# Performance work log

Hardware: AMD Instinct MI355X
Metric: run time of the kernel (lower is better)

The kernel has to match this reference:

```python
import jax, jax.numpy as jnp
import numpy as np

D_MODEL = 512
NHEAD = 8
MAX_REL = 256  # max_relative_position


def _linear(x, w, b):
    # torch nn.Linear: y = x @ W^T + b, W: [out, in]
    return jnp.einsum('...i,oi->...o', x, w) + b


def setup_inputs() -> dict:
    key = jax.random.key(0)
    ks = jax.random.split(key, 16)
    B, S, D = 32, 512, D_MODEL
    s = 0.02
    inp = {
        'query': jax.random.normal(ks[0], (B, S, D), jnp.float32),
        'key':   jax.random.normal(ks[1], (B, S, D), jnp.float32),
        'value': jax.random.normal(ks[2], (B, S, D), jnp.float32),
        # local attention projections (torch Linear weights [out,in])
        'wq': jax.random.normal(ks[3], (D, D), jnp.float32) * s,
        'bq': jnp.zeros((D,), jnp.float32),
        'wk': jax.random.normal(ks[4], (D, D), jnp.float32) * s,
        'bk': jnp.zeros((D,), jnp.float32),
        'wv': jax.random.normal(ks[5], (D, D), jnp.float32) * s,
        'bv': jnp.zeros((D,), jnp.float32),
        'wo': jax.random.normal(ks[6], (D, D), jnp.float32) * s,
        'bo': jnp.zeros((D,), jnp.float32),
        # relative-position key embedding table [2*MAX_REL+1, head_dim]
        'rel_k': jax.random.normal(ks[7], (2 * MAX_REL + 1, D // NHEAD), jnp.float32) * s,
        # global nn.MultiheadAttention (nhead//2 heads): packed in_proj + out_proj
        'g_in_w': jax.random.normal(ks[8], (3 * D, D), jnp.float32) * s,
        'g_in_b': jnp.zeros((3 * D,), jnp.float32),
        'g_out_w': jax.random.normal(ks[9], (D, D), jnp.float32) * s,
        'g_out_b': jnp.zeros((D,), jnp.float32),
    }
    return inp


def reference(query, key, value, wq, bq, wk, bk, wv, bv, wo, bo, rel_k,
              g_in_w, g_in_b, g_out_w, g_out_b):
    B, S, D = query.shape
    H, hd = NHEAD, D // NHEAD

    # --- local attention with relative-position bias ---
    q = _linear(query, wq, bq).reshape(B, S, H, hd).transpose(0, 2, 1, 3)  # [B,H,S,hd]
    k = _linear(key,   wk, bk).reshape(B, S, H, hd).transpose(0, 2, 1, 3)
    v = _linear(value, wv, bv).reshape(B, S, H, hd).transpose(0, 2, 1, 3)

    scores = jnp.einsum('bhqd,bhkd->bhqk', q, k) / jnp.sqrt(jnp.float32(hd))

    # relative positions: distance[i,j] = j - i, clamped, shifted to [0, 2*MAX_REL]
    idx = jnp.arange(S)
    rel_ids = jnp.clip(idx[None, :] - idx[:, None], -MAX_REL, MAX_REL) + MAX_REL  # [S,S]
    rel_pos_k = rel_k[rel_ids]  # [S, S, hd]
    scores = scores + jnp.einsum('bhld,lrd->bhlr', q, rel_pos_k)

    attn = jax.nn.softmax(scores, axis=-1)
    local = jnp.einsum('bhqk,bhkd->bhqd', attn, v)
    local = local.transpose(0, 2, 1, 3).reshape(B, S, D)

    # --- global MHA with H//2 heads ---
    Hg = H // 2
    hdg = D // Hg
    qg = _linear(query, g_in_w[:D], g_in_b[:D]).reshape(B, S, Hg, hdg).transpose(0, 2, 1, 3)
    kg = _linear(key,   g_in_w[D:2 * D], g_in_b[D:2 * D]).reshape(B, S, Hg, hdg).transpose(0, 2, 1, 3)
    vg = _linear(value, g_in_w[2 * D:], g_in_b[2 * D:]).reshape(B, S, Hg, hdg).transpose(0, 2, 1, 3)
    gs = jnp.einsum('bhqd,bhkd->bhqk', qg, kg) / jnp.sqrt(jnp.float32(hdg))
    ga = jax.nn.softmax(gs, axis=-1)
    g = jnp.einsum('bhqk,bhkd->bhqd', ga, vg).transpose(0, 2, 1, 3).reshape(B, S, D)
    g = _linear(g, g_out_w, g_out_b)

    combined = 0.7 * local + 0.3 * g
    return _linear(combined, wo, bo)
```

## Files before the change

kernel.cpp:

```cpp
#include <hip/hip_runtime.h>

typedef __attribute__((ext_vector_type(8))) short bh8;
typedef __attribute__((ext_vector_type(4))) float f4;

#define DEVI static __device__ __forceinline__

DEVI unsigned short f2b(float f) {
  union { float f; unsigned u; } v; v.f = f;
  unsigned r = v.u + 0x7fffu + ((v.u >> 16) & 1u);
  return (unsigned short)(r >> 16);
}
DEVI float b2f(unsigned short h) {
  union { unsigned u; float f; } v; v.u = ((unsigned)h) << 16;
  return v.f;
}
DEVI f4 mfma16(bh8 a, bh8 b, f4 c) {
  return __builtin_amdgcn_mfma_f32_16x16x32_bf16(a, b, c, 0, 0, 0);
}
DEVI void gload_lds16(const unsigned short* g, unsigned short* l) {
  __builtin_amdgcn_global_load_lds(
      (const __attribute__((address_space(1))) void*)(g),
      (__attribute__((address_space(3))) void*)(l), 16, 0, 0);
}

__global__ __launch_bounds__(256) void prep_x_kern(
    const float* __restrict__ q, const float* __restrict__ k, const float* __restrict__ v,
    unsigned short* __restrict__ xq, unsigned short* __restrict__ xk, unsigned short* __restrict__ xv) {
  long i = ((long)blockIdx.x * 256 + threadIdx.x) * 4;
  if (i >= 8388608L) return;
  float4 a = *(const float4*)(q + i);
  float4 b = *(const float4*)(k + i);
  float4 c = *(const float4*)(v + i);
  union { unsigned short s[4]; uint2 u; } pa, pb, pc;
  pa.s[0] = f2b(a.x); pa.s[1] = f2b(a.y); pa.s[2] = f2b(a.z); pa.s[3] = f2b(a.w);
  pb.s[0] = f2b(b.x); pb.s[1] = f2b(b.y); pb.s[2] = f2b(b.z); pb.s[3] = f2b(b.w);
  pc.s[0] = f2b(c.x); pc.s[1] = f2b(c.y); pc.s[2] = f2b(c.z); pc.s[3] = f2b(c.w);
  *(uint2*)(xq + i) = pa.u;
  *(uint2*)(xk + i) = pb.u;
  *(uint2*)(xv + i) = pc.u;
}

__global__ __launch_bounds__(256) void prep_w_kern(
    const float* __restrict__ wq, const float* __restrict__ wk, const float* __restrict__ wv,
    const float* __restrict__ g_in_w, const float* __restrict__ g_out_w,
    const float* __restrict__ wo, const float* __restrict__ rel_k,
    unsigned short* __restrict__ Wq, unsigned short* __restrict__ Wk, unsigned short* __restrict__ Wv,
    unsigned short* __restrict__ Wgo, unsigned short* __restrict__ Wo_, unsigned short* __restrict__ Rk) {
  long i = ((long)blockIdx.x * 256 + threadIdx.x) * 4;
  if (i >= 2129984L) return;
  const float* src; unsigned short* dst; long off;
  if (i < 524288L)        { dst = Wq;  off = i; src = (i < 262144L) ? wq + i : g_in_w + (i - 262144L); }
  else if (i < 1048576L)  { long j = i - 524288L;  dst = Wk;  off = j; src = (j < 262144L) ? wk + j : g_in_w + j; }
  else if (i < 1572864L)  { long j = i - 1048576L; dst = Wv;  off = j; src = (j < 262144L) ? wv + j : g_in_w + 262144L + j; }
  else if (i < 1835008L)  { long j = i - 1572864L; dst = Wgo; off = j; src = g_out_w + j; }
  else if (i < 2097152L)  { long j = i - 1835008L; dst = Wo_; off = j; src = wo + j; }
  else                    { long j = i - 2097152L; dst = Rk;  off = j; src = rel_k + j; }
  float4 f = *(const float4*)src;
  union { unsigned short s[4]; uint2 u; } p;
  p.s[0] = f2b(f.x); p.s[1] = f2b(f.y); p.s[2] = f2b(f.z); p.s[3] = f2b(f.w);
  *(uint2*)(dst + off) = p.u;
}

template <int NB, int EPI>
__global__ __launch_bounds__(256) void gemm_bf16_kern(
    const unsigned short* __restrict__ A, const unsigned short* __restrict__ Bw,
    const float* __restrict__ bias0, const float* __restrict__ bias1,
    const unsigned short* __restrict__ aux,
    unsigned short* __restrict__ outb, unsigned short* __restrict__ outb2,
    float* __restrict__ outf) {
  __shared__ unsigned short lsA[128 * 32];
  __shared__ unsigned short lsB[128 * 32];
  const int t = threadIdx.x;
  const int lane = t & 63, w = t >> 6;
  const int l15 = lane & 15, g8 = (lane >> 4) * 8, g4 = (lane >> 4) * 4;
  int n = blockIdx.x;
  int x = n >> 3, c = n & 7;
  const int rb = (c * 16 + (x & 15)) * 128;
  const int cb = (x >> 4) * 128;
  const int wr = (w >> 1) * 64, wc = (w & 1) * 64;
  const int e0 = t * 8, e1 = 2048 + t * 8;
  const int r0 = e0 >> 5, k0i = e0 & 31;
  const int r1 = e1 >> 5, k1i = e1 & 31;

  const unsigned short* pa0 = A + (long)(rb + r0) * 512 + k0i;
  const unsigned short* pa1 = A + (long)(rb + r1) * 512 + k1i;
  const unsigned short* pb0 = Bw + (long)(cb + r0) * 512 + k0i;
  const unsigned short* pb1 = Bw + (long)(cb + r1) * 512 + k1i;
  unsigned short* dA0 = lsA + w * 512;
  unsigned short* dA1 = lsA + 2048 + w * 512;
  unsigned short* dB0 = lsB + w * 512;
  unsigned short* dB1 = lsB + 2048 + w * 512;

  f4 acc[4][4] = {};
  for (int k0 = 0; k0 < 512; k0 += 32) {
    __syncthreads();
    gload_lds16(pa0 + k0, dA0);
    gload_lds16(pa1 + k0, dA1);
    gload_lds16(pb0 + k0, dB0);
    gload_lds16(pb1 + k0, dB1);
    __syncthreads();
    bh8 af[4], bf[4];
#pragma unroll
    for (int m = 0; m < 4; m++) af[m] = *(const bh8*)(lsA + (wr + m * 16 + l15) * 32 + g8);
#pragma unroll
    for (int nn = 0; nn < 4; nn++) bf[nn] = *(const bh8*)(lsB + (wc + nn * 16 + l15) * 32 + g8);
#pragma unroll
    for (int m = 0; m < 4; m++)
#pragma unroll
      for (int nn = 0; nn < 4; nn++)
        acc[m][nn] = mfma16(af[m], bf[nn], acc[m][nn]);
  }
#pragma unroll
  for (int m = 0; m < 4; m++) {
#pragma unroll
    for (int nn = 0; nn < 4; nn++) {
      if constexpr (EPI == 3) {
        int col = cb + wc + nn * 16 + l15;
        float bsv = (col < 512) ? bias0[col] : bias1[col - 512];
        unsigned r[4];
#pragma unroll
        for (int j = 0; j < 4; j++) {
          union { float f; unsigned u; } v; v.f = acc[m][nn][j] + bsv;
          r[j] = v.u + 0x7fffu + ((v.u >> 16) & 1u);
        }
        unsigned lo = (r[0] >> 16) | (r[1] & 0xffff0000u);
        unsigned hi = (r[2] >> 16) | (r[3] & 0xffff0000u);
        int row0 = rb + wr + m * 16 + g4;
        int bb = row0 >> 9, s = row0 & 511;
        if (col < 512) {
          int hh = col >> 6, d = col & 63;
          *(uint2*)(outb + (((long)(bb * 8 + hh) * 64 + d) << 9) + s) = make_uint2(lo, hi);
        } else {
          int c2 = col - 512, hg = c2 >> 7, dg = c2 & 127;
          *(uint2*)(outb2 + (((long)(bb * 4 + hg) * 128 + dg) << 9) + s) = make_uint2(lo, hi);
        }
      } else {
#pragma unroll
        for (int j = 0; j < 4; j++) {
          int row = rb + wr + m * 16 + g4 + j;
          int col = cb + wc + nn * 16 + l15;
          float v = acc[m][nn][j];
          if constexpr (EPI == 0) {
            v += (col < 512) ? bias0[col] : bias1[col - 512];
            outb[(long)row * (NB * 128) + col] = f2b(v);
          } else if constexpr (EPI == 1) {
            v += bias0[col];
            float cv = 0.7f * b2f(aux[(long)row * 512 + col]) + 0.3f * v;
            outb[(long)row * 512 + col] = f2b(cv);
          } else {
            v += bias0[col];
            outf[(long)row * 512 + col] = v;
          }
        }
      }
    }
  }
}

__global__ __launch_bounds__(512, 4) void attn_local_kern(
    const unsigned short* __restrict__ Yq, const unsigned short* __restrict__ Yk,
    const unsigned short* __restrict__ Yvt, const unsigned short* __restrict__ relk,
    unsigned short* __restrict__ outL) {
  __shared__ unsigned short kv[2][8192];
  __shared__ unsigned short buf[32 * 524];
  __shared__ float redbuf[8][32];

  const int t = threadIdx.x, lane = t & 63, w = t >> 6;
  const int l15 = lane & 15, g = lane >> 4, g8 = g * 8;
  int n = blockIdx.x;
  int bid = (n & 7) * 512 + (n >> 3);
  const int qt = bid & 15;
  const int h = (bid >> 4) & 7;
  const int b = bid >> 7;
  const int qb = qt * 32;
  const long base = ((long)(b * 512)) * 1024 + h * 64;
  const long vbase = ((long)(b * 8 + h)) * 64 * 512;

#define STAGE_K(ROFF, BUF) { \
    const int c_ = t & 7; \
    _Pragma("unroll") \
    for (int it = 0; it < 2; it++) { \
      int rr = it * 64 + (t >> 3); \
      gload_lds16(Yk + base + (long)((ROFF) + rr) * 1024 + ((c_ ^ (rr & 7)) * 8), \
                  kv[BUF] + it * 4096 + w * 512); \
    } }
#define STAGE_V(COFF, BUF) { \
    const int c_ = t & 15; \
    _Pragma("unroll") \
    for (int it = 0; it < 2; it++) { \
      int dd_ = it * 32 + (t >> 4); \
      gload_lds16(Yvt + vbase + (long)dd_ * 512 + (COFF) + ((c_ ^ (dd_ & 15)) * 8), \
                  kv[BUF] + it * 4096 + w * 512); \
    } }

#define QK(CH) { \
    int rl = w * 16 + l15; \
    const unsigned short* kb_ = kv[(CH) & 1]; \
    bh8 k0 = *(const bh8*)(kb_ + rl * 64 + ((g ^ (rl & 7)) * 8)); \
    bh8 k1 = *(const bh8*)(kb_ + rl * 64 + (((g + 4) ^ (rl & 7)) * 8)); \
    _Pragma("unroll") \
    for (int mm = 0; mm < 2; mm++) { \
      f4 a = {}; \
      a = mfma16(qf[mm][0], k0, a); \
      a = mfma16(qf[mm][1], k1, a); \
      sc[mm][CH] = a; \
    } }

#define GATHER(CH) { \
    _Pragma("unroll") \
    for (int mm = 0; mm < 2; mm++) \
    _Pragma("unroll") \
    for (int j = 0; j < 4; j++) { \
      int lr = mm * 16 + g * 4 + j; \
      int rowb = lr * 524; \
      int idx = rowb + 256 - (qb + lr) + (CH) * 128 + w * 16 + l15; \
      idx = idx < rowb ? rowb : idx; \
      idx = idx > rowb + 512 ? rowb + 512 : idx; \
      float p = exp2f(fmaf(sc[mm][CH][j], 0.18033688011112042f, b2f(buf[idx]))); \
      sc[mm][CH][j] = p; \
      rs[mm][j] += p; \
    } }

  STAGE_K(0, 0);

  bh8 qf[2][2];
#pragma unroll
  for (int mm = 0; mm < 2; mm++) {
    const unsigned short* qp = Yq + base + (long)(qb + mm * 16 + l15) * 1024 + g8;
    qf[mm][0] = *(const bh8*)(qp);
    qf[mm][1] = *(const bh8*)(qp + 32);
  }

  for (int tt = w; tt < 33; tt += 8) {
    int ri = tt * 16 + l15; if (ri > 512) ri = 512;
    const unsigned short* rp = relk + ri * 64 + g8;
    bh8 rf0 = *(const bh8*)(rp), rf1 = *(const bh8*)(rp + 32);
    int col = tt * 16 + l15;
#pragma unroll
    for (int mm = 0; mm < 2; mm++) {
      f4 a = {};
      a = mfma16(qf[mm][0], rf0, a);
      a = mfma16(qf[mm][1], rf1, a);
      if (col < 524) {
#pragma unroll
        for (int j = 0; j < 4; j++)
          buf[(mm * 16 + g * 4 + j) * 524 + col] = f2b(a[j] * 1.4426950408889634f);
      }
    }
  }
  __syncthreads();

  f4 sc[2][4];
  float rs[2][4] = {};

#pragma unroll
  for (int c = 0; c < 4; c++) {
    if (c < 3) { STAGE_K((c + 1) * 128, (c + 1) & 1); }
    else       { STAGE_V(0, 0); }
    __builtin_amdgcn_s_setprio(1);
    QK(c);
    __builtin_amdgcn_s_setprio(0);
    GATHER(c);
    __syncthreads();
  }

#pragma unroll
  for (int mm = 0; mm < 2; mm++)
#pragma unroll
    for (int j = 0; j < 4; j++) {
      int lr = mm * 16 + g * 4 + j;
      float s = rs[mm][j];
      for (int d = 1; d < 16; d <<= 1) s += __shfl_xor(s, d, 64);
      if (l15 == 0) redbuf[w][lr] = s;
    }
#pragma unroll
  for (int mm = 0; mm < 2; mm++)
#pragma unroll
    for (int ch = 0; ch < 4; ch++) {
      int col = ch * 128 + w * 16 + l15;
#pragma unroll
      for (int j = 0; j < 4; j++)
        buf[(mm * 16 + g * 4 + j) * 524 + col] = f2b(sc[mm][ch][j]);
    }
  __syncthreads();

  const int mmw = w >> 2, dt = w & 3;
  const int dd = dt * 16 + l15;
  float rinvj[4];
#pragma unroll
  for (int j = 0; j < 4; j++) {
    int lr = mmw * 16 + g * 4 + j;
    float s = 0.f;
#pragma unroll
    for (int ww = 0; ww < 8; ww++) s += redbuf[ww][lr];
    rinvj[j] = __builtin_amdgcn_rcpf(s);
  }

  f4 accO = {};
#pragma unroll
  for (int d = 0; d < 4; d++) {
    if (d < 3) { STAGE_V((d + 1) * 128, (d + 1) & 1); }
    const unsigned short* vb_ = kv[d & 1];
    __builtin_amdgcn_s_setprio(1);
#pragma unroll
    for (int ks2 = 0; ks2 < 4; ks2++) {
      union { uint2 u[2]; bh8 v; } pa;
      const unsigned short* pp = buf + (mmw * 16 + l15) * 524 + (d * 4 + ks2) * 32 + g8;
      pa.u[0] = *(const uint2*)(pp);
      pa.u[1] = *(const uint2*)(pp + 4);
      bh8 vv = *(const bh8*)(vb_ + dd * 128 + (((ks2 * 4 + g) ^ (dd & 15)) * 8));
      accO = mfma16(pa.v, vv, accO);
    }
    __builtin_amdgcn_s_setprio(0);
    if (d < 3) __syncthreads();
  }
#pragma unroll
  for (int j = 0; j < 4; j++) {
    int row = qb + mmw * 16 + g * 4 + j;
    outL[((long)(b * 512 + row)) * 512 + h * 64 + dt * 16 + l15] = f2b(accO[j] * rinvj[j]);
  }
#undef STAGE_K
#undef STAGE_V
#undef QK
#undef GATHER
}

__global__ __launch_bounds__(512) void attn_glob_kern(
    const unsigned short* __restrict__ Yq, const unsigned short* __restrict__ Yk,
    const unsigned short* __restrict__ Yvt, unsigned short* __restrict__ outG) {
  __shared__ unsigned short buf[32 * 520];
  __shared__ float redbuf[8][32];

  const int t = threadIdx.x, lane = t & 63, w = t >> 6;
  const int l15 = lane & 15, g = lane >> 4, g8 = g * 8;
  int n = blockIdx.x;
  int bid = (n & 7) * 256 + (n >> 3);
  const int qt = bid & 15;
  const int hg = (bid >> 4) & 3;
  const int b = bid >> 6;
  const int qb = qt * 32;
  const long base = ((long)(b * 512)) * 1024 + 512 + hg * 128;

  bh8 qf[2][4];
#pragma unroll
  for (int mm = 0; mm < 2; mm++) {
    const unsigned short* qp = Yq + base + (long)(qb + mm * 16 + l15) * 1024 + g8;
#pragma unroll
    for (int ks = 0; ks < 4; ks++) qf[mm][ks] = *(const bh8*)(qp + ks * 32);
  }

  f4 sc[2][4];
  __builtin_amdgcn_s_setprio(1);
#pragma unroll
  for (int ct = 0; ct < 4; ct++) {
    int r = w * 64 + ct * 16 + l15;
    const unsigned short* kp = Yk + base + (long)r * 1024 + g8;
    bh8 kf[4];
#pragma unroll
    for (int ks = 0; ks < 4; ks++) kf[ks] = *(const bh8*)(kp + ks * 32);
#pragma unroll
    for (int mm = 0; mm < 2; mm++) {
      f4 a = {};
#pragma unroll
      for (int ks = 0; ks < 4; ks++) a = mfma16(qf[mm][ks], kf[ks], a);
      sc[mm][ct] = a;
    }
  }
  __builtin_amdgcn_s_setprio(0);

#pragma unroll
  for (int mm = 0; mm < 2; mm++) {
#pragma unroll
    for (int j = 0; j < 4; j++) {
      int lr = mm * 16 + g * 4 + j;
      float s = 0.f;
#pragma unroll
      for (int ct = 0; ct < 4; ct++) {
        float p = exp2f(sc[mm][ct][j] * 0.12751745334f);
        sc[mm][ct][j] = p;
        s += p;
      }
      for (int d = 1; d < 16; d <<= 1) s += __shfl_xor(s, d, 64);
      if (l15 == 0) redbuf[w][lr] = s;
    }
  }
#pragma unroll
  for (int mm = 0; mm < 2; mm++)
#pragma unroll
    for (int ct = 0; ct < 4; ct++) {
      int col = w * 64 + ct * 16 + l15;
#pragma unroll
      for (int j = 0; j < 4; j++)
        buf[(mm * 16 + g * 4 + j) * 520 + col] = f2b(sc[mm][ct][j]);
    }
  __syncthreads();

  float rinv[2][4];
#pragma unroll
  for (int mm = 0; mm < 2; mm++)
#pragma unroll
    for (int j = 0; j < 4; j++) {
      int lr = mm * 16 + g * 4 + j;
      float s = 0.f;
#pragma unroll
      for (int ww = 0; ww < 8; ww++) s += redbuf[ww][lr];
      rinv[mm][j] = __builtin_amdgcn_rcpf(s);
    }

  f4 accO[2] = {};
  const unsigned short* vr = Yvt + ((long)(b * 4 + hg) * 128 + w * 16 + l15) * 512;
  __builtin_amdgcn_s_setprio(1);
#pragma unroll
  for (int ks = 0; ks < 16; ks++) {
    bh8 vb = *(const bh8*)(vr + ks * 32 + g8);
#pragma unroll
    for (int mm = 0; mm < 2; mm++) {
      union { uint2 u[2]; bh8 v; } pa;
      const unsigned short* pp = buf + (mm * 16 + l15) * 520 + ks * 32 + g8;
      pa.u[0] = *(const uint2*)(pp);
      pa.u[1] = *(const uint2*)(pp + 4);
      accO[mm] = mfma16(pa.v, vb, accO[mm]);
    }
  }
  __builtin_amdgcn_s_setprio(0);
#pragma unroll
  for (int mm = 0; mm < 2; mm++)
#pragma unroll
    for (int j = 0; j < 4; j++) {
      int row = qb + mm * 16 + g * 4 + j;
      outG[((long)(b * 512 + row)) * 512 + hg * 128 + w * 16 + l15] = f2b(accO[mm][j] * rinv[mm][j]);
    }
}

extern "C" void kernel_launch(void* const* d_in, const int* in_sizes, int n_in,
                              void* d_out, int out_size, void* d_ws, size_t ws_size,
                              hipStream_t stream) {
  const float* query = (const float*)d_in[0];
  const float* key   = (const float*)d_in[1];
  const float* value = (const float*)d_in[2];
  const float* wq = (const float*)d_in[3];   const float* bq = (const float*)d_in[4];
  const float* wk = (const float*)d_in[5];   const float* bk = (const float*)d_in[6];
  const float* wv = (const float*)d_in[7];   const float* bv = (const float*)d_in[8];
  const float* wo = (const float*)d_in[9];   const float* bo = (const float*)d_in[10];
  const float* rel_k = (const float*)d_in[11];
  const float* g_in_w = (const float*)d_in[12];  const float* g_in_b = (const float*)d_in[13];
  const float* g_out_w = (const float*)d_in[14]; const float* g_out_b = (const float*)d_in[15];

  unsigned short* p = (unsigned short*)d_ws;
  unsigned short* Xq = p;            p += 8388608;
  unsigned short* Xk = p;            p += 8388608;
  unsigned short* Xv = p;            p += 8388608;
  unsigned short* Yq = p;            p += 16777216;
  unsigned short* Yk = p;            p += 16777216;
  unsigned short* Yvt_l = p;         p += 8388608;
  unsigned short* Yvt_g = p;         p += 8388608;
  unsigned short* Wq = p;            p += 524288;
  unsigned short* Wk = p;            p += 524288;
  unsigned short* Wv = p;            p += 524288;
  unsigned short* Wgo = p;           p += 262144;
  unsigned short* Wo_ = p;           p += 262144;
  unsigned short* Rk = p;            p += 32832;
  unsigned short* localb = Xq;
  unsigned short* gattnb = Xk;
  unsigned short* comb   = Xv;

  prep_x_kern<<<8192, 256, 0, stream>>>(query, key, value, Xq, Xk, Xv);
  prep_w_kern<<<2081, 256, 0, stream>>>(wq, wk, wv, g_in_w, g_out_w, wo, rel_k,
                                        Wq, Wk, Wv, Wgo, Wo_, Rk);

  gemm_bf16_kern<8, 0><<<1024, 256, 0, stream>>>(Xq, Wq, bq, g_in_b, nullptr, Yq, nullptr, nullptr);
  gemm_bf16_kern<8, 0><<<1024, 256, 0, stream>>>(Xk, Wk, bk, g_in_b + 512, nullptr, Yk, nullptr, nullptr);
  gemm_bf16_kern<8, 3><<<1024, 256, 0, stream>>>(Xv, Wv, bv, g_in_b + 1024, nullptr, Yvt_l, Yvt_g, nullptr);

  attn_local_kern<<<4096, 512, 0, stream>>>(Yq, Yk, Yvt_l, Rk, localb);
  attn_glob_kern<<<2048, 512, 0, stream>>>(Yq, Yk, Yvt_g, gattnb);

  gemm_bf16_kern<4, 1><<<512, 256, 0, stream>>>(gattnb, Wgo, g_out_b, nullptr, localb, comb, nullptr, nullptr);
  gemm_bf16_kern<4, 2><<<512, 256, 0, stream>>>(comb, Wo_, bo, nullptr, nullptr, nullptr, nullptr, (float*)d_out);
}
```

Measured before the change: 339.7 us.

## Fold global out-projection into final projection via precomputed combined weight

Precomputes Wo·0.3·Wgo as a bf16 weight on device and concatenates it with 0.7·Wo into a K=1024 weight. The attention kernels write local and global outputs side by side into one buffer, so a single K=1024 GEMM replaces the two chained 512-K GEMMs. The combined bias is folded in by a small kernel. This removes an intermediate write and read plus one launch, at the cost of a small weight-product GEMM per call and an extra bf16 rounding of the fused weight.

New measurement: 361.1 us. 1.06x slower.

```diff
diff --git a/kernel.cpp b/kernel.cpp
--- a/kernel.cpp
+++ b/kernel.cpp
@@ -45,27 +45,53 @@
     const float* __restrict__ g_in_w, const float* __restrict__ g_out_w,
     const float* __restrict__ wo, const float* __restrict__ rel_k,
     unsigned short* __restrict__ Wq, unsigned short* __restrict__ Wk, unsigned short* __restrict__ Wv,
-    unsigned short* __restrict__ Wgo, unsigned short* __restrict__ Wo_, unsigned short* __restrict__ Rk) {
+    unsigned short* __restrict__ Wo_, unsigned short* __restrict__ WgoT,
+    unsigned short* __restrict__ Bfin, unsigned short* __restrict__ Rk) {
   long i = ((long)blockIdx.x * 256 + threadIdx.x) * 4;
-  if (i >= 2129984L) return;
-  const float* src; unsigned short* dst; long off;
+  if (i >= 2392128L) return;
+  if (i >= 2097152L && i < 2359296L) {
+    long off = i - 2097152L;
+    int ii = (int)(off >> 9), p = (int)(off & 511);
+    union { unsigned short s[4]; uint2 u; } w;
+#pragma unroll
+    for (int tt = 0; tt < 4; tt++) w.s[tt] = f2b(g_out_w[(p + tt) * 512 + ii]);
+    *(uint2*)(WgoT + off) = w.u;
+    return;
+  }
+  const float* src; unsigned short* dst; long off; float sc = 1.0f;
   if (i < 524288L)        { dst = Wq;  off = i; src = (i < 262144L) ? wq + i : g_in_w + (i - 262144L); }
   else if (i < 1048576L)  { long j = i - 524288L;  dst = Wk;  off = j; src = (j < 262144L) ? wk + j : g_in_w + j; }
   else if (i < 1572864L)  { long j = i - 1048576L; dst = Wv;  off = j; src = (j < 262144L) ? wv + j : g_in_w + 262144L + j; }
-  else if (i < 1835008L)  { long j = i - 1572864L; dst = Wgo; off = j; src = g_out_w + j; }
-  else if (i < 2097152L)  { long j = i - 1835008L; dst = Wo_; off = j; src = wo + j; }
-  else                    { long j = i - 2097152L; dst = Rk;  off = j; src = rel_k + j; }
+  else if (i < 1835008L)  { long j = i - 1572864L; dst = Wo_; off = j; src = wo + j; }
+  else if (i < 2097152L)  { long j = i - 1835008L; int col = (int)(j >> 9), k = (int)(j & 511);
+                            dst = Bfin; off = (long)col * 1024 + k; src = wo + j; sc = 0.7f; }
+  else                    { long j = i - 2359296L; dst = Rk;  off = j; src = rel_k + j; }
   float4 f = *(const float4*)src;
   union { unsigned short s[4]; uint2 u; } p;
-  p.s[0] = f2b(f.x); p.s[1] = f2b(f.y); p.s[2] = f2b(f.z); p.s[3] = f2b(f.w);
+  p.s[0] = f2b(f.x * sc); p.s[1] = f2b(f.y * sc); p.s[2] = f2b(f.z * sc); p.s[3] = f2b(f.w * sc);
   *(uint2*)(dst + off) = p.u;
 }
 
-template <int NB, int EPI>
+__global__ __launch_bounds__(256) void bias2_kern(
+    const float* __restrict__ wo, const float* __restrict__ bgo,
+    const float* __restrict__ bo, float* __restrict__ bias2) {
+  int o = blockIdx.x * 256 + threadIdx.x;
+  if (o >= 512) return;
+  const float* r = wo + (long)o * 512;
+  float s = 0.f;
+#pragma unroll 4
+  for (int m = 0; m < 512; m += 4) {
+    float4 a = *(const float4*)(r + m);
+    float4 b = *(const float4*)(bgo + m);
+    s += a.x * b.x + a.y * b.y + a.z * b.z + a.w * b.w;
+  }
+  bias2[o] = bo[o] + 0.3f * s;
+}
+
+template <int NB, int EPI, int KD, int LDA, int GRIDM>
 __global__ __launch_bounds__(256) void gemm_bf16_kern(
     const unsigned short* __restrict__ A, const unsigned short* __restrict__ Bw,
     const float* __restrict__ bias0, const float* __restrict__ bias1,
-    const unsigned short* __restrict__ aux,
     unsigned short* __restrict__ outb, unsigned short* __restrict__ outb2,
     float* __restrict__ outf) {
   __shared__ unsigned short lsA[128 * 32];
@@ -74,25 +100,30 @@
   const int lane = t & 63, w = t >> 6;
   const int l15 = lane & 15, g8 = (lane >> 4) * 8, g4 = (lane >> 4) * 4;
   int n = blockIdx.x;
-  int x = n >> 3, c = n & 7;
-  const int rb = (c * 16 + (x & 15)) * 128;
-  const int cb = (x >> 4) * 128;
+  int rb, cb;
+  if constexpr (GRIDM > 0) {
+    rb = (n % GRIDM) * 128; cb = (n / GRIDM) * 128;
+  } else {
+    int x = n >> 3, c = n & 7;
+    rb = (c * 16 + (x & 15)) * 128;
+    cb = (x >> 4) * 128;
+  }
   const int wr = (w >> 1) * 64, wc = (w & 1) * 64;
   const int e0 = t * 8, e1 = 2048 + t * 8;
   const int r0 = e0 >> 5, k0i = e0 & 31;
   const int r1 = e1 >> 5, k1i = e1 & 31;
 
-  const unsigned short* pa0 = A + (long)(rb + r0) * 512 + k0i;
-  const unsigned short* pa1 = A + (long)(rb + r1) * 512 + k1i;
-  const unsigned short* pb0 = Bw + (long)(cb + r0) * 512 + k0i;
-  const unsigned short* pb1 = Bw + (long)(cb + r1) * 512 + k1i;
+  const unsigned short* pa0 = A + (long)(rb + r0) * LDA + k0i;
+  const unsigned short* pa1 = A + (long)(rb + r1) * LDA + k1i;
+  const unsigned short* pb0 = Bw + (long)(cb + r0) * KD + k0i;
+  const unsigned short* pb1 = Bw + (long)(cb + r1) * KD + k1i;
   unsigned short* dA0 = lsA + w * 512;
   unsigned short* dA1 = lsA + 2048 + w * 512;
   unsigned short* dB0 = lsB + w * 512;
   unsigned short* dB1 = lsB + 2048 + w * 512;
 
   f4 acc[4][4] = {};
-  for (int k0 = 0; k0 < 512; k0 += 32) {
+  for (int k0 = 0; k0 < KD; k0 += 32) {
     __syncthreads();
     gload_lds16(pa0 + k0, dA0);
     gload_lds16(pa1 + k0, dA1);
@@ -143,10 +174,8 @@
           if constexpr (EPI == 0) {
             v += (col < 512) ? bias0[col] : bias1[col - 512];
             outb[(long)row * (NB * 128) + col] = f2b(v);
-          } else if constexpr (EPI == 1) {
-            v += bias0[col];
-            float cv = 0.7f * b2f(aux[(long)row * 512 + col]) + 0.3f * v;
-            outb[(long)row * 512 + col] = f2b(cv);
+          } else if constexpr (EPI == 5) {
+            outb[(long)row * 1024 + 512 + col] = f2b(0.3f * v);
           } else {
             v += bias0[col];
             outf[(long)row * 512 + col] = v;
@@ -160,7 +189,7 @@
 __global__ __launch_bounds__(512, 4) void attn_local_kern(
     const unsigned short* __restrict__ Yq, const unsigned short* __restrict__ Yk,
     const unsigned short* __restrict__ Yvt, const unsigned short* __restrict__ relk,
-    unsigned short* __restrict__ outL) {
+    unsigned short* __restrict__ outC) {
   __shared__ unsigned short kv[2][8192];
   __shared__ unsigned short buf[32 * 524];
   __shared__ float redbuf[8][32];
@@ -192,7 +221,6 @@
       gload_lds16(Yvt + vbase + (long)dd_ * 512 + (COFF) + ((c_ ^ (dd_ & 15)) * 8), \
                   kv[BUF] + it * 4096 + w * 512); \
     } }
-
 #define QK(CH) { \
     int rl = w * 16 + l15; \
     const unsigned short* kb_ = kv[(CH) & 1]; \
@@ -205,7 +233,6 @@
       a = mfma16(qf[mm][1], k1, a); \
       sc[mm][CH] = a; \
     } }
-
 #define GATHER(CH) { \
     _Pragma("unroll") \
     for (int mm = 0; mm < 2; mm++) \
@@ -317,7 +344,7 @@
 #pragma unroll
   for (int j = 0; j < 4; j++) {
     int row = qb + mmw * 16 + g * 4 + j;
-    outL[((long)(b * 512 + row)) * 512 + h * 64 + dt * 16 + l15] = f2b(accO[j] * rinvj[j]);
+    outC[((long)(b * 512 + row)) * 1024 + h * 64 + dt * 16 + l15] = f2b(accO[j] * rinvj[j]);
   }
 #undef STAGE_K
 #undef STAGE_V
@@ -327,7 +354,7 @@
 
 __global__ __launch_bounds__(512) void attn_glob_kern(
     const unsigned short* __restrict__ Yq, const unsigned short* __restrict__ Yk,
-    const unsigned short* __restrict__ Yvt, unsigned short* __restrict__ outG) {
+    const unsigned short* __restrict__ Yvt, unsigned short* __restrict__ outC) {
   __shared__ unsigned short buf[32 * 520];
   __shared__ float redbuf[8][32];
 
@@ -428,7 +455,7 @@
 #pragma unroll
     for (int j = 0; j < 4; j++) {
       int row = qb + mm * 16 + g * 4 + j;
-      outG[((long)(b * 512 + row)) * 512 + hg * 128 + w * 16 + l15] = f2b(accO[mm][j] * rinv[mm][j]);
+      outC[((long)(b * 512 + row)) * 1024 + 512 + hg * 128 + w * 16 + l15] = f2b(accO[mm][j] * rinv[mm][j]);
     }
 }
 
@@ -457,24 +484,28 @@
   unsigned short* Wq = p;            p += 524288;
   unsigned short* Wk = p;            p += 524288;
   unsigned short* Wv = p;            p += 524288;
-  unsigned short* Wgo = p;           p += 262144;
   unsigned short* Wo_ = p;           p += 262144;
+  unsigned short* WgoT = p;          p += 262144;
+  unsigned short* Bfin = p;          p += 524288;
   unsigned short* Rk = p;            p += 32832;
-  unsigned short* localb = Xq;
-  unsigned short* gattnb = Xk;
-  unsigned short* comb   = Xv;
+  float* bias2 = (float*)p;          p += 1024;
+  unsigned short* CAT = Xq;
 
   prep_x_kern<<<8192, 256, 0, stream>>>(query, key, value, Xq, Xk, Xv);
-  prep_w_kern<<<2081, 256, 0, stream>>>(wq, wk, wv, g_in_w, g_out_w, wo, rel_k,
-                                        Wq, Wk, Wv, Wgo, Wo_, Rk);
-
-  gemm_bf16_kern<8, 0><<<1024, 256, 0, stream>>>(Xq, Wq, bq, g_in_b, nullptr, Yq, nullptr, nullptr);
-  gemm_bf16_kern<8, 0><<<1024, 256, 0, stream>>>(Xk, Wk, bk, g_in_b + 512, nullptr, Yk, nullptr, nullptr);
-  gemm_bf16_kern<8, 3><<<1024, 256, 0, stream>>>(Xv, Wv, bv, g_in_b + 1024, nullptr, Yvt_l, Yvt_g, nullptr);
-
-  attn_local_kern<<<4096, 512, 0, stream>>>(Yq, Yk, Yvt_l, Rk, localb);
-  attn_glob_kern<<<2048, 512, 0, stream>>>(Yq, Yk, Yvt_g, gattnb);
-
-  gemm_bf16_kern<4, 1><<<512, 256, 0, stream>>>(gattnb, Wgo, g_out_b, nullptr, localb, comb, nullptr, nullptr);
-  gemm_bf16_kern<4, 2><<<512, 256, 0, stream>>>(comb, Wo_, bo, nullptr, nullptr, nullptr, nullptr, (float*)d_out);
-}
+  prep_w_kern<<<2337, 256, 0, stream>>>(wq, wk, wv, g_in_w, g_out_w, wo, rel_k,
+                                        Wq, Wk, Wv, Wo_, WgoT, Bfin, Rk);
+  bias2_kern<<<2, 256, 0, stream>>>(wo, g_out_b, bo, bias2);
+
+  gemm_bf16_kern<4, 5, 512, 512, 4><<<16, 256, 0, stream>>>(
+      Wo_, WgoT, nullptr, nullptr, Bfin, nullptr, nullptr);
+
+  gemm_bf16_kern<8, 0, 512, 512, 0><<<1024, 256, 0, stream>>>(Xq, Wq, bq, g_in_b, Yq, nullptr, nullptr);
+  gemm_bf16_kern<8, 0, 512, 512, 0><<<1024, 256, 0, stream>>>(Xk, Wk, bk, g_in_b + 512, Yk, nullptr, nullptr);
+  gemm_bf16_kern<8, 3, 512, 512, 0><<<1024, 256, 0, stream>>>(Xv, Wv, bv, g_in_b + 1024, Yvt_l, Yvt_g, nullptr);
+
+  attn_local_kern<<<4096, 512, 0, stream>>>(Yq, Yk, Yvt_l, Rk, CAT);
+  attn_glob_kern<<<2048, 512, 0, stream>>>(Yq, Yk, Yvt_g, CAT);
+
+  gemm_bf16_kern<4, 2, 1024, 1024, 0><<<512, 256, 0, stream>>>(
+      CAT, Bfin, bias2, nullptr, nullptr, nullptr, (float*)d_out);
+}
```
